# Kernel tuning notes

Hardware: AMD Instinct MI355X
Metric: run time of the kernel (lower is better)

Reference implementation:

```python
import jax, jax.numpy as jnp
import numpy as np
import math

BS, C, NH, NL, NP = 2, 128, 1, 2, 8
SHAPES = np.array([[128, 256], [64, 128]], dtype=np.int64)  # [num_level, (H, W)]
NQ = int(SHAPES[0, 0] * SHAPES[0, 1])  # 32768 queries at level-0 resolution
NV = int((SHAPES[:, 0] * SHAPES[:, 1]).sum())  # 40960


def _offset_bias():
    # replicate init_weights grid bias
    thetas = np.arange(NH, dtype=np.float32) * (2.0 * math.pi / NH)
    grid = np.stack([np.cos(thetas), np.sin(thetas)], -1)
    grid = grid / np.abs(grid).max(-1, keepdims=True)
    grid = np.tile(grid.reshape(NH, 1, 1, 2), (1, NL, NP, 1))
    for i in range(NP):
        grid[:, :, i, :] *= i + 1
    return jnp.asarray(grid.reshape(-1), dtype=jnp.float32)


def setup_inputs() -> dict:
    key = jax.random.key(0)
    ks = jax.random.split(key, 8)
    query = jax.random.normal(ks[0], (BS, NQ, C), dtype=jnp.float32)
    value = jax.random.normal(ks[1], (BS, NV, C), dtype=jnp.float32)
    query_location = jax.random.uniform(ks[2], (BS, NQ, NL, 2), dtype=jnp.float32)
    spatial_shapes = jnp.asarray(SHAPES)
    level_start_index = jnp.asarray(np.concatenate([[0], np.cumsum(SHAPES[:, 0] * SHAPES[:, 1])[:-1]]))
    # params (small random offset weights instead of exact-zero init so offsets depend on query)
    W_off = 0.01 * jax.random.normal(ks[3], (C, NH * NL * NP * 2), dtype=jnp.float32)
    b_off = _offset_bias()
    W_attn = 0.01 * jax.random.normal(ks[4], (C, NH * NL * NP), dtype=jnp.float32)
    b_attn = jnp.zeros((NH * NL * NP,), dtype=jnp.float32)
    lim = 1.0 / np.sqrt(C)
    W_out = jax.random.uniform(ks[5], (C * NH, C), minval=-lim, maxval=lim, dtype=jnp.float32)
    b_out = jnp.zeros((C,), dtype=jnp.float32)
    return {"query": query, "value": value, "query_location": query_location,
            "spatial_shapes": spatial_shapes, "level_start_index": level_start_index,
            "W_off": W_off, "b_off": b_off, "W_attn": W_attn, "b_attn": b_attn,
            "W_out": W_out, "b_out": b_out}


def _ms_deform_attn(value, shapes_np, loc, aw):
    # value: [bs, nv, c]; loc: [bs, nq, nh, nl, np, 2] in [0,1]; aw: [bs, nq, nh, nl, np]
    bs, nq = loc.shape[0], loc.shape[1]
    hd = value.shape[-1] // NH
    out = jnp.zeros((bs, NH, nq, hd), dtype=value.dtype)
    start = 0
    for l in range(NL):
        H, W = int(shapes_np[l, 0]), int(shapes_np[l, 1])
        # [bs, nh, H*W, hd]
        v = value[:, start:start + H * W].reshape(bs, H * W, NH, hd).transpose(0, 2, 1, 3)
        # grid_sample align_corners=False convention: x = gx*W - 0.5 with gx in [0,1]
        x = loc[:, :, :, l, :, 0] * W - 0.5  # [bs, nq, nh, np]
        y = loc[:, :, :, l, :, 1] * H - 0.5
        x0 = jnp.floor(x); y0 = jnp.floor(y)
        lx = (x - x0).transpose(0, 2, 1, 3).reshape(bs, NH, nq * NP)[..., None]
        ly = (y - y0).transpose(0, 2, 1, 3).reshape(bs, NH, nq * NP)[..., None]
        x0i = x0.astype(jnp.int32); y0i = y0.astype(jnp.int32)

        def gat(ix, iy):
            valid = ((ix >= 0) & (ix < W) & (iy >= 0) & (iy < H)).astype(value.dtype)
            idx = jnp.clip(iy, 0, H - 1) * W + jnp.clip(ix, 0, W - 1)
            idx_t = idx.transpose(0, 2, 1, 3).reshape(bs, NH, nq * NP)
            g = jnp.take_along_axis(v, idx_t[..., None], axis=2)  # [bs, nh, nq*np, hd]
            m = valid.transpose(0, 2, 1, 3).reshape(bs, NH, nq * NP)
            return g * m[..., None]

        samp = (gat(x0i, y0i) * (1 - lx) * (1 - ly)
                + gat(x0i + 1, y0i) * lx * (1 - ly)
                + gat(x0i, y0i + 1) * (1 - lx) * ly
                + gat(x0i + 1, y0i + 1) * lx * ly)  # [bs, nh, nq*np, hd]
        w = aw[:, :, :, l].transpose(0, 2, 1, 3).reshape(bs, NH, nq * NP)[..., None]
        out = out + (samp * w).reshape(bs, NH, nq, NP, hd).sum(3)
        start += H * W
    return out.transpose(0, 2, 1, 3).reshape(bs, nq, NH * hd)


def reference(query, value, query_location, spatial_shapes, level_start_index,
              W_off, b_off, W_attn, b_attn, W_out, b_out):
    bs, nq, c = query.shape
    shapes_np = np.asarray(spatial_shapes)
    off = (query @ W_off + b_off).reshape(bs, nq, NH, NL, NP, 2)
    aw = jax.nn.softmax((query @ W_attn + b_attn).reshape(bs, nq, NH, NL * NP), axis=-1)
    aw = aw.reshape(bs, nq, NH, NL, NP)
    # offset_normalizer = [W, H] per level
    norm = jnp.stack([jnp.asarray(shapes_np[:, 1], jnp.float32),
                      jnp.asarray(shapes_np[:, 0], jnp.float32)], -1)  # [nl, 2]
    loc = query_location[:, :, None, :, None, :] + off / norm[None, None, None, :, None, :]
    out = _ms_deform_attn(value, shapes_np, loc, aw)
    return out @ W_out + b_out  # dropout is identity at eval
```

## Files before the change

kernel.cpp:

```cpp
#include <hip/hip_runtime.h>
#include <hip/hip_fp16.h>


#define QB 32

struct __align__(8) h2x2 { __half2 a, b; };

typedef _Float16 f16x8 __attribute__((ext_vector_type(8)));
typedef _Float16 f16x4 __attribute__((ext_vector_type(4)));
typedef float    f32x4 __attribute__((ext_vector_type(4)));

__global__ __launch_bounds__(256) void cvt_value_f16_kernel(
    const float4* __restrict__ in, h2x2* __restrict__ out, int n4)
{
    const int i = blockIdx.x * 256 + threadIdx.x;
    if (i < n4) {
        const float4 f = in[i];
        h2x2 h;
        h.a = __floats2half2_rn(f.x, f.y);
        h.b = __floats2half2_rn(f.z, f.w);
        out[i] = h;
    }
}

__global__ __launch_bounds__(256) void wout_transpose_kernel(
    const float* __restrict__ Wout, _Float16* __restrict__ wTg)
{
    __shared__ float t[128 * 129];
    const int tid = threadIdx.x;
    #pragma unroll
    for (int i = 0; i < 16; ++i) {
        const int f  = tid + i * 256;
        const int k  = f >> 5;
        const int c4 = f & 31;
        const float4 v = ((const float4*)Wout)[k * 32 + c4];
        t[k * 129 + c4 * 4 + 0] = v.x;
        t[k * 129 + c4 * 4 + 1] = v.y;
        t[k * 129 + c4 * 4 + 2] = v.z;
        t[k * 129 + c4 * 4 + 3] = v.w;
    }
    __syncthreads();
    #pragma unroll
    for (int i = 0; i < 64; ++i) {
        const int f = tid + i * 256;
        const int n = f >> 7;
        const int k = f & 127;
        wTg[n * 128 + k] = (_Float16)t[k * 129 + n];
    }
}

#define MSDA_PROLOGUE                                                          \
    float* q_tile = (float*)smem_u;                                            \
    int4*  tab    = (int4*)smem_u;                                             \
    const int tid = threadIdx.x;                                               \
    const int r0  = blockIdx.x * QB;                                           \
    {                                                                          \
        const float4* src = (const float4*)query + (size_t)r0 * 32;            \
        float4* dst = (float4*)q_tile;                                         \
        _Pragma("unroll")                                                      \
        for (int i = 0; i < 4; ++i)                                            \
            dst[tid + i * 256] = src[tid + i * 256];                           \
    }                                                                          \
    __syncthreads();                                                           \
    {                                                                          \
        const int jo = tid & 31;                                               \
        const int qb = (tid >> 5) * 4;                                         \
        float s[4] = {0.f, 0.f, 0.f, 0.f};                                     \
        for (int c4 = 0; c4 < 32; ++c4) {                                      \
            const float w0 = Woff[(c4 * 4 + 0) * 32 + jo];                     \
            const float w1 = Woff[(c4 * 4 + 1) * 32 + jo];                     \
            const float w2 = Woff[(c4 * 4 + 2) * 32 + jo];                     \
            const float w3 = Woff[(c4 * 4 + 3) * 32 + jo];                     \
            _Pragma("unroll")                                                  \
            for (int k = 0; k < 4; ++k) {                                      \
                const float4 q4 = *(const float4*)&q_tile[(qb + k) * 128 + c4 * 4]; \
                s[k] += q4.x * w0 + q4.y * w1 + q4.z * w2 + q4.w * w3;         \
            }                                                                  \
        }                                                                      \
        const int l = jo >> 4;                                                 \
        const int d = jo & 1;                                                  \
        const float scale = (d == 0) ? (l == 0 ? 256.f : 128.f)                \
                                     : (l == 0 ? 128.f : 64.f);                \
        const float bo = boff[jo];                                             \
        _Pragma("unroll")                                                      \
        for (int k = 0; k < 4; ++k) {                                          \
            const int row = r0 + qb + k;                                       \
            const float ql = qloc[row * 4 + l * 2 + d];                        \
            coords[(qb + k) * 32 + jo] = ql * scale + (s[k] + bo) - 0.5f;      \
        }                                                                      \
    }                                                                          \
    {                                                                          \
        const int ja = tid & 15;                                               \
        const int qb = (tid >> 4) * 2;                                         \
        float s[2] = {0.f, 0.f};                                               \
        for (int c4 = 0; c4 < 32; ++c4) {                                      \
            const float w0 = Wattn[(c4 * 4 + 0) * 16 + ja];                    \
            const float w1 = Wattn[(c4 * 4 + 1) * 16 + ja];                    \
            const float w2 = Wattn[(c4 * 4 + 2) * 16 + ja];                    \
            const float w3 = Wattn[(c4 * 4 + 3) * 16 + ja];                    \
            _Pragma("unroll")                                                  \
            for (int k = 0; k < 2; ++k) {                                      \
                const float4 q4 = *(const float4*)&q_tile[(qb + k) * 128 + c4 * 4]; \
                s[k] += q4.x * w0 + q4.y * w1 + q4.z * w2 + q4.w * w3;         \
            }                                                                  \
        }                                                                      \
        const float ba = battn[ja];                                            \
        _Pragma("unroll")                                                      \
        for (int k = 0; k < 2; ++k)                                            \
            aws[(qb + k) * 16 + ja] = s[k] + ba;                               \
    }                                                                          \
    __syncthreads();                                                           \
    if (tid < QB) {                                                            \
        float* a = &aws[tid * 16];                                             \
        float m = a[0];                                                        \
        _Pragma("unroll")                                                      \
        for (int j = 1; j < 16; ++j) m = fmaxf(m, a[j]);                       \
        float sum = 0.f;                                                       \
        _Pragma("unroll")                                                      \
        for (int j = 0; j < 16; ++j) {                                         \
            const float e = __expf(a[j] - m);                                  \
            a[j] = e;                                                          \
            sum += e;                                                          \
        }                                                                      \
        const float r = 1.f / sum;                                             \
        _Pragma("unroll")                                                      \
        for (int j = 0; j < 16; ++j) a[j] *= r;                                \
    }                                                                          \
    __syncthreads();                                                           \
    _Pragma("unroll")                                                          \
    for (int e = tid; e < QB * 16; e += 256) {                                 \
        const int q = e >> 4;                                                  \
        const int p = e & 15;                                                  \
        const int l = p >> 3;                                                  \
        const int H = l ? 64 : 128;                                            \
        const int W = l ? 128 : 256;                                           \
        const int S = l ? 32768 : 0;                                           \
        const float x   = coords[q * 32 + p * 2 + 0];                          \
        const float y   = coords[q * 32 + p * 2 + 1];                          \
        const float wgt = aws[q * 16 + p];                                     \
        const float xf = floorf(x), yf = floorf(y);                            \
        const float lx = x - xf, ly = y - yf;                                  \
        const int x0 = (int)xf, y0 = (int)yf;                                  \
        const int x1 = x0 + 1, y1 = y0 + 1;                                    \
        const float hx = 1.f - lx, hy = 1.f - ly;                              \
        float w00 = wgt * hx * hy;                                             \
        float w10 = wgt * lx * hy;                                             \
        float w01 = wgt * hx * ly;                                             \
        float w11 = wgt * lx * ly;                                             \
        if (x0 < 0 || x0 >= W) { w00 = 0.f; w01 = 0.f; }                       \
        if (x1 < 0 || x1 >= W) { w10 = 0.f; w11 = 0.f; }                       \
        if (y0 < 0 || y0 >= H) { w00 = 0.f; w10 = 0.f; }                       \
        if (y1 < 0 || y1 >= H) { w01 = 0.f; w11 = 0.f; }                       \
        const int cx0 = min(max(x0, 0), W - 1);                                \
        const int cx1 = min(max(x1, 0), W - 1);                                \
        const int cy0 = min(max(y0, 0), H - 1);                                \
        const int cy1 = min(max(y1, 0), H - 1);                                \
        int4 e0, e1;                                                           \
        e0.x = __float_as_int(w00); e0.y = __float_as_int(w01);                \
        e0.z = (S + cy0 * W + cx0) * 32; e0.w = (S + cy1 * W + cx0) * 32;      \
        e1.x = __float_as_int(w10); e1.y = __float_as_int(w11);                \
        e1.z = (S + cy0 * W + cx1) * 32; e1.w = (S + cy1 * W + cx1) * 32;      \
        tab[e * 2]     = e0;                                                   \
        tab[e * 2 + 1] = e1;                                                   \
    }                                                                          \
    __syncthreads();

__global__ __launch_bounds__(256, 4) void msda_gather_f16_kernel(
    const float* __restrict__ query,
    const h2x2*  __restrict__ value_h,
    const float* __restrict__ qloc,
    const float* __restrict__ Woff,
    const float* __restrict__ boff,
    const float* __restrict__ Wattn,
    const float* __restrict__ battn,
    float* __restrict__ acc_out)
{
    __shared__ __align__(16) char smem_u[QB * 128 * 4];
    __shared__ float coords[QB * 32];
    __shared__ float aws[QB * 16];
    MSDA_PROLOGUE

    {
        const int wv   = tid >> 6;
        const int lane = tid & 63;
        const int half = lane >> 5;
        const int cl   = lane & 31;
        const h2x2* vb = value_h + (size_t)(blockIdx.x >> 10) * (40960 * 32);
        float4* og = (float4*)acc_out;

        #pragma unroll 1
        for (int i = 0; i < 8; ++i) {
            const int q = wv * 8 + i;
            float ax = 0.f, ay = 0.f, az = 0.f, aw4 = 0.f;

            #pragma unroll 1
            for (int p0 = 0; p0 < 16; p0 += 8) {
                float wa[8], wb[8];
                int   oa[8], ob[8];
                #pragma unroll
                for (int pi = 0; pi < 8; ++pi) {
                    const int4 t = tab[((q * 16 + p0 + pi) << 1) + half];
                    wa[pi] = __int_as_float(t.x);
                    wb[pi] = __int_as_float(t.y);
                    oa[pi] = t.z + cl;
                    ob[pi] = t.w + cl;
                }
                h2x2 vA[8], vB[8];
                #pragma unroll
                for (int pi = 0; pi < 8; ++pi) {
                    vA[pi] = vb[oa[pi]];
                    vB[pi] = vb[ob[pi]];
                }
                #pragma unroll
                for (int pi = 0; pi < 8; ++pi) {
                    ax  += wa[pi] * __low2float(vA[pi].a);
                    ay  += wa[pi] * __high2float(vA[pi].a);
                    az  += wa[pi] * __low2float(vA[pi].b);
                    aw4 += wa[pi] * __high2float(vA[pi].b);
                    ax  += wb[pi] * __low2float(vB[pi].a);
                    ay  += wb[pi] * __high2float(vB[pi].a);
                    az  += wb[pi] * __low2float(vB[pi].b);
                    aw4 += wb[pi] * __high2float(vB[pi].b);
                }
            }
            ax  += __shfl_xor(ax, 32, 64);
            ay  += __shfl_xor(ay, 32, 64);
            az  += __shfl_xor(az, 32, 64);
            aw4 += __shfl_xor(aw4, 32, 64);
            if (half == 0)
                og[(size_t)(r0 + q) * 32 + cl] = make_float4(ax, ay, az, aw4);
        }
    }
}

__global__ __launch_bounds__(256, 4) void msda_gather_f32_kernel(
    const float* __restrict__ query,
    const float* __restrict__ value,
    const float* __restrict__ qloc,
    const float* __restrict__ Woff,
    const float* __restrict__ boff,
    const float* __restrict__ Wattn,
    const float* __restrict__ battn,
    float* __restrict__ acc_out)
{
    __shared__ __align__(16) char smem_u[QB * 128 * 4];
    __shared__ float coords[QB * 32];
    __shared__ float aws[QB * 16];
    MSDA_PROLOGUE

    {
        const int wv   = tid >> 6;
        const int lane = tid & 63;
        const int half = lane >> 5;
        const int cl   = lane & 31;
        const float4* vb = (const float4*)value
                         + (size_t)(blockIdx.x >> 10) * (40960 * 32);
        float4* og = (float4*)acc_out;

        #pragma unroll 1
        for (int i = 0; i < 8; ++i) {
            const int q = wv * 8 + i;
            float ax = 0.f, ay = 0.f, az = 0.f, aw4 = 0.f;

            #pragma unroll 1
            for (int p0 = 0; p0 < 16; p0 += 8) {
                float wa[8], wb[8];
                int   oa[8], ob[8];
                #pragma unroll
                for (int pi = 0; pi < 8; ++pi) {
                    const int4 t = tab[((q * 16 + p0 + pi) << 1) + half];
                    wa[pi] = __int_as_float(t.x);
                    wb[pi] = __int_as_float(t.y);
                    oa[pi] = t.z + cl;
                    ob[pi] = t.w + cl;
                }
                float4 vA[8], vB[8];
                #pragma unroll
                for (int pi = 0; pi < 8; ++pi) {
                    vA[pi] = vb[oa[pi]];
                    vB[pi] = vb[ob[pi]];
                }
                #pragma unroll
                for (int pi = 0; pi < 8; ++pi) {
                    ax  += wa[pi] * vA[pi].x + wb[pi] * vB[pi].x;
                    ay  += wa[pi] * vA[pi].y + wb[pi] * vB[pi].y;
                    az  += wa[pi] * vA[pi].z + wb[pi] * vB[pi].z;
                    aw4 += wa[pi] * vA[pi].w + wb[pi] * vB[pi].w;
                }
            }
            ax  += __shfl_xor(ax, 32, 64);
            ay  += __shfl_xor(ay, 32, 64);
            az  += __shfl_xor(az, 32, 64);
            aw4 += __shfl_xor(aw4, 32, 64);
            if (half == 0)
                og[(size_t)(r0 + q) * 32 + cl] = make_float4(ax, ay, az, aw4);
        }
    }
}

__global__ __launch_bounds__(256, 2) void msda_out_gemm_mfma_kernel(
    const _Float16* __restrict__ wTg,
    const float* __restrict__ bout,
    float* __restrict__ out)
{
    __shared__ _Float16 aT[128 * 136];
    __shared__ _Float16 wT[128 * 136];
    const int tid = threadIdx.x;
    const int m0  = blockIdx.x * 128;

    #pragma unroll
    for (int i = 0; i < 8; ++i) {
        const int t  = tid + i * 256;
        const int n  = t >> 4;
        const int k8 = t & 15;
        *(f16x8*)&wT[n * 136 + k8 * 8] = *(const f16x8*)&wTg[n * 128 + k8 * 8];
    }
    {
        const float4* src = (const float4*)out;
        #pragma unroll
        for (int i = 0; i < 16; ++i) {
            const int t  = tid + i * 256;
            const int r  = t >> 5;
            const int c4 = t & 31;
            const float4 v = src[(size_t)(m0 + r) * 32 + c4];
            f16x4 h;
            h[0] = (_Float16)v.x; h[1] = (_Float16)v.y;
            h[2] = (_Float16)v.z; h[3] = (_Float16)v.w;
            *(f16x4*)&aT[r * 136 + c4 * 4] = h;
        }
    }
    __syncthreads();

    const int wv   = tid >> 6;
    const int lane = tid & 63;
    const int quad = lane >> 4;
    const int lr   = lane & 15;

    f32x4 acc_[2][8];
    #pragma unroll
    for (int mt = 0; mt < 2; ++mt)
        #pragma unroll
        for (int nt = 0; nt < 8; ++nt)
            acc_[mt][nt] = (f32x4){0.f, 0.f, 0.f, 0.f};

    #pragma unroll
    for (int k0 = 0; k0 < 128; k0 += 32) {
        const f16x8 a0 = *(const f16x8*)&aT[(wv * 32 +  0 + lr) * 136 + k0 + quad * 8];
        const f16x8 a1 = *(const f16x8*)&aT[(wv * 32 + 16 + lr) * 136 + k0 + quad * 8];
        #pragma unroll
        for (int nt = 0; nt < 8; ++nt) {
            const f16x8 b = *(const f16x8*)&wT[(nt * 16 + lr) * 136 + k0 + quad * 8];
            acc_[0][nt] = __builtin_amdgcn_mfma_f32_16x16x32_f16(a0, b, acc_[0][nt], 0, 0, 0);
            acc_[1][nt] = __builtin_amdgcn_mfma_f32_16x16x32_f16(a1, b, acc_[1][nt], 0, 0, 0);
        }
    }

    #pragma unroll
    for (int nt = 0; nt < 8; ++nt) {
        const float bb = bout[nt * 16 + lr];
        #pragma unroll
        for (int mt = 0; mt < 2; ++mt) {
            #pragma unroll
            for (int reg = 0; reg < 4; ++reg) {
                const int row = m0 + wv * 32 + mt * 16 + quad * 4 + reg;
                out[(size_t)row * 128 + nt * 16 + lr] = acc_[mt][nt][reg] + bb;
            }
        }
    }
}

#define GR 128
__global__ __launch_bounds__(256, 2) void msda_out_gemm_f32_kernel(
    const float* __restrict__ Wout,
    const float* __restrict__ bout,
    float* __restrict__ out)
{
    __shared__ __align__(16) float a_tile[GR * 68];
    __shared__ __align__(16) float w_tile[64 * 128];
    const int tid  = threadIdx.x;
    const int r0   = blockIdx.x * GR;
    const int trow = tid >> 4;
    const int tcol = tid & 15;

    float4 o[8][2];
    #pragma unroll
    for (int k = 0; k < 8; ++k) {
        o[k][0] = make_float4(0.f, 0.f, 0.f, 0.f);
        o[k][1] = make_float4(0.f, 0.f, 0.f, 0.f);
    }

    #pragma unroll 1
    for (int h = 0; h < 2; ++h) {
        {
            const float4* src = (const float4*)out;
            #pragma unroll
            for (int i = 0; i < 8; ++i) {
                const int t  = tid + i * 256;
                const int r  = t >> 4;
                const int c4 = t & 15;
                const float4 v = src[(size_t)(r0 + r) * 32 + h * 16 + c4];
                *(float4*)&a_tile[r * 68 + c4 * 4] = v;
            }
            const float4* ws = (const float4*)Wout + (size_t)h * 64 * 32;
            float4* wd = (float4*)w_tile;
            #pragma unroll
            for (int i = 0; i < 8; ++i)
                wd[tid + i * 256] = ws[tid + i * 256];
        }
        __syncthreads();

        #pragma unroll 1
        for (int c4 = 0; c4 < 16; ++c4) {
            float4 a4[8];
            #pragma unroll
            for (int k = 0; k < 8; ++k)
                a4[k] = *(const float4*)&a_tile[(trow + 16 * k) * 68 + c4 * 4];
            #pragma unroll
            for (int j = 0; j < 4; ++j) {
                const int ci = c4 * 4 + j;
                const float4 w0 = *(const float4*)&w_tile[ci * 128 + tcol * 4];
                const float4 w1 = *(const float4*)&w_tile[ci * 128 + 64 + tcol * 4];
                #pragma unroll
                for (int k = 0; k < 8; ++k) {
                    const float a = (j == 0) ? a4[k].x : (j == 1) ? a4[k].y
                                  : (j == 2) ? a4[k].z : a4[k].w;
                    o[k][0].x += a * w0.x; o[k][0].y += a * w0.y;
                    o[k][0].z += a * w0.z; o[k][0].w += a * w0.w;
                    o[k][1].x += a * w1.x; o[k][1].y += a * w1.y;
                    o[k][1].z += a * w1.z; o[k][1].w += a * w1.w;
                }
            }
        }
        __syncthreads();
    }

    const float4 b0 = ((const float4*)bout)[tcol];
    const float4 b1 = ((const float4*)bout)[16 + tcol];
    float4* og = (float4*)out;
    #pragma unroll
    for (int k = 0; k < 8; ++k) {
        const size_t row = (size_t)(r0 + trow + 16 * k);
        float4 v0 = o[k][0], v1 = o[k][1];
        v0.x += b0.x; v0.y += b0.y; v0.z += b0.z; v0.w += b0.w;
        v1.x += b1.x; v1.y += b1.y; v1.z += b1.z; v1.w += b1.w;
        og[row * 32 + tcol]      = v0;
        og[row * 32 + 16 + tcol] = v1;
    }
}

extern "C" void kernel_launch(void* const* d_in, const int* in_sizes, int n_in,
                              void* d_out, int out_size, void* d_ws, size_t ws_size,
                              hipStream_t stream) {
    const float* query = (const float*)d_in[0];
    const float* value = (const float*)d_in[1];
    const float* qloc  = (const float*)d_in[2];
    const float* Woff  = (const float*)d_in[5];
    const float* boff  = (const float*)d_in[6];
    const float* Wattn = (const float*)d_in[7];
    const float* battn = (const float*)d_in[8];
    const float* Wout  = (const float*)d_in[9];
    const float* bout  = (const float*)d_in[10];
    float* out = (float*)d_out;

    const int n_val = 2 * 40960 * 128;
    const size_t f16_bytes = (size_t)n_val * 2;
    const size_t wT_bytes  = 128 * 128 * 2;

    if (ws_size >= f16_bytes + wT_bytes) {
        h2x2* val16 = (h2x2*)d_ws;
        _Float16* wTg = (_Float16*)((char*)d_ws + f16_bytes);
        const int n4 = n_val / 4;
        hipLaunchKernelGGL(cvt_value_f16_kernel, dim3((n4 + 255) / 256), dim3(256),
                           0, stream, (const float4*)value, val16, n4);
        hipLaunchKernelGGL(wout_transpose_kernel, dim3(1), dim3(256), 0, stream,
                           Wout, wTg);
        hipLaunchKernelGGL(msda_gather_f16_kernel, dim3(65536 / QB), dim3(256),
                           0, stream,
                           query, (const h2x2*)val16, qloc, Woff, boff, Wattn, battn, out);
        hipLaunchKernelGGL(msda_out_gemm_mfma_kernel, dim3(65536 / 128), dim3(256),
                           0, stream, (const _Float16*)wTg, bout, out);
    } else if (ws_size >= f16_bytes) {
        h2x2* val16 = (h2x2*)d_ws;
        const int n4 = n_val / 4;
        hipLaunchKernelGGL(cvt_value_f16_kernel, dim3((n4 + 255) / 256), dim3(256),
                           0, stream, (const float4*)value, val16, n4);
        hipLaunchKernelGGL(msda_gather_f16_kernel, dim3(65536 / QB), dim3(256),
                           0, stream,
                           query, (const h2x2*)val16, qloc, Woff, boff, Wattn, battn, out);
        hipLaunchKernelGGL(msda_out_gemm_f32_kernel, dim3(65536 / GR), dim3(256),
                           0, stream, Wout, bout, out);
    } else {
        hipLaunchKernelGGL(msda_gather_f32_kernel, dim3(65536 / QB), dim3(256),
                           0, stream,
                           query, value, qloc, Woff, boff, Wattn, battn, out);
        hipLaunchKernelGGL(msda_out_gemm_f32_kernel, dim3(65536 / GR), dim3(256),
                           0, stream, Wout, bout, out);
    }
}
```

Baseline: 225.6 us.

## Fuse offset, attention-logit and softmax projections into one register pass with shuffles

```diff
diff --git a/kernel.cpp b/kernel.cpp
--- a/kernel.cpp
+++ b/kernel.cpp
@@ -63,109 +63,96 @@
     }                                                                          \
     __syncthreads();                                                           \
     {                                                                          \
-        const int jo = tid & 31;                                               \
-        const int qb = (tid >> 5) * 4;                                         \
-        float s[4] = {0.f, 0.f, 0.f, 0.f};                                     \
+        const int qg  = tid >> 4;                   \
+        const int p   = tid & 15;                      \
+        const int l   = p >> 3;                                                \
+        const int pin = p & 7;                                                 \
+        const int jx  = l * 16 + pin * 2;      \
+        float sx[2] = {0.f, 0.f}, sy[2] = {0.f, 0.f}, sa[2] = {0.f, 0.f};      \
         for (int c4 = 0; c4 < 32; ++c4) {                                      \
-            const float w0 = Woff[(c4 * 4 + 0) * 32 + jo];                     \
-            const float w1 = Woff[(c4 * 4 + 1) * 32 + jo];                     \
-            const float w2 = Woff[(c4 * 4 + 2) * 32 + jo];                     \
-            const float w3 = Woff[(c4 * 4 + 3) * 32 + jo];                     \
+            float2 wxy[4]; float wat[4];                                       \
             _Pragma("unroll")                                                  \
-            for (int k = 0; k < 4; ++k) {                                      \
-                const float4 q4 = *(const float4*)&q_tile[(qb + k) * 128 + c4 * 4]; \
-                s[k] += q4.x * w0 + q4.y * w1 + q4.z * w2 + q4.w * w3;         \
+            for (int r = 0; r < 4; ++r) {                                      \
+                wxy[r] = *(const float2*)&Woff[(c4 * 4 + r) * 32 + jx];        \
+                wat[r] = Wattn[(c4 * 4 + r) * 16 + p];                         \
+            }                                                                  \
+            _Pragma("unroll")                                                  \
+            for (int k = 0; k < 2; ++k) {                                      \
+                const float4 q4 = *(const float4*)&q_tile[(qg * 2 + k) * 128 + c4 * 4]; \
+                sx[k] += q4.x * wxy[0].x + q4.y * wxy[1].x                     \
+                       + q4.z * wxy[2].x + q4.w * wxy[3].x;                    \
+                sy[k] += q4.x * wxy[0].y + q4.y * wxy[1].y                     \
+                       + q4.z * wxy[2].y + q4.w * wxy[3].y;                    \
+                sa[k] += q4.x * wat[0] + q4.y * wat[1]                         \
+                       + q4.z * wat[2] + q4.w * wat[3];                        \
             }                                                                  \
         }                                                                      \
-        const int l = jo >> 4;                                                 \
-        const int d = jo & 1;                                                  \
-        const float scale = (d == 0) ? (l == 0 ? 256.f : 128.f)                \
-                                     : (l == 0 ? 128.f : 64.f);                \
-        const float bo = boff[jo];                                             \
+        const float Wf = l ? 128.f : 256.f;                                    \
+        const float Hf = l ? 64.f : 128.f;                                     \
+        const float box = boff[jx], boy = boff[jx + 1];                        \
+        const float ba  = battn[p];                                            \
+        float xx[2], yy[2], lg[2];                                             \
         _Pragma("unroll")                                                      \
-        for (int k = 0; k < 4; ++k) {                                          \
-            const int row = r0 + qb + k;                                       \
-            const float ql = qloc[row * 4 + l * 2 + d];                        \
-            coords[(qb + k) * 32 + jo] = ql * scale + (s[k] + bo) - 0.5f;      \
+        for (int k = 0; k < 2; ++k) {                                          \
+            const int row = r0 + qg * 2 + k;                                   \
+            xx[k] = qloc[row * 4 + l * 2 + 0] * Wf + (sx[k] + box) - 0.5f;     \
+            yy[k] = qloc[row * 4 + l * 2 + 1] * Hf + (sy[k] + boy) - 0.5f;     \
+            lg[k] = sa[k] + ba;                                                \
+        }                                                                      \
+                  \
+        float m0 = lg[0], m1 = lg[1];                                          \
+        _Pragma("unroll")                                                      \
+        for (int s_ = 1; s_ < 16; s_ <<= 1) {                                  \
+            m0 = fmaxf(m0, __shfl_xor(m0, s_, 64));                            \
+            m1 = fmaxf(m1, __shfl_xor(m1, s_, 64));                            \
+        }                                                                      \
+        float ex0 = __expf(lg[0] - m0), ex1 = __expf(lg[1] - m1);              \
+        float sm0 = ex0, sm1 = ex1;                                            \
+        _Pragma("unroll")                                                      \
+        for (int s_ = 1; s_ < 16; s_ <<= 1) {                                  \
+            sm0 += __shfl_xor(sm0, s_, 64);                                    \
+            sm1 += __shfl_xor(sm1, s_, 64);                                    \
+        }                                                                      \
+        const float wgt_[2] = {ex0 / sm0, ex1 / sm1};                          \
+        __syncthreads();    \
+        const int Hi = l ? 64 : 128;                                           \
+        const int Wi = l ? 128 : 256;                                          \
+        const int S  = l ? 32768 : 0;                                          \
+        _Pragma("unroll")                                                      \
+        for (int k = 0; k < 2; ++k) {                                          \
+            const int q = qg * 2 + k;                                          \
+            const float x = xx[k], y = yy[k];                                  \
+            const float wgt = wgt_[k];                                         \
+            const float xf = floorf(x), yf = floorf(y);                        \
+            const float lx = x - xf, ly = y - yf;                              \
+            const int x0 = (int)xf, y0 = (int)yf;                              \
+            const int x1 = x0 + 1, y1 = y0 + 1;                                \
+            const float hx = 1.f - lx, hy = 1.f - ly;                          \
+            float w00 = wgt * hx * hy;                                         \
+            float w10 = wgt * lx * hy;                                         \
+            float w01 = wgt * hx * ly;                                         \
+            float w11 = wgt * lx * ly;                                         \
+            if (x0 < 0 || x0 >= Wi) { w00 = 0.f; w01 = 0.f; }                  \
+            if (x1 < 0 || x1 >= Wi) { w10 = 0.f; w11 = 0.f; }                  \
+            if (y0 < 0 || y0 >= Hi) { w00 = 0.f; w10 = 0.f; }                  \
+            if (y1 < 0 || y1 >= Hi) { w01 = 0.f; w11 = 0.f; }                  \
+            const int cx0 = min(max(x0, 0), Wi - 1);                           \
+            const int cx1 = min(max(x1, 0), Wi - 1);                           \
+            const int cy0 = min(max(y0, 0), Hi - 1);                           \
+            const int cy1 = min(max(y1, 0), Hi - 1);                           \
+            int4 e0i, e1i;                                                     \
+            e0i.x = __float_as_int(w00); e0i.y = __float_as_int(w01);          \
+            e0i.z = (S + cy0 * Wi + cx0) * 32; e0i.w = (S + cy1 * Wi + cx0) * 32; \
+            e1i.x = __float_as_int(w10); e1i.y = __float_as_int(w11);          \
+            e1i.z = (S + cy0 * Wi + cx1) * 32; e1i.w = (S + cy1 * Wi + cx1) * 32; \
+            const int e_ = q * 16 + p;                                         \
+            tab[e_ * 2]     = e0i;                                             \
+            tab[e_ * 2 + 1] = e1i;                                             \
         }                                                                      \
     }                                                                          \
-    {                                                                          \
-        const int ja = tid & 15;                                               \
-        const int qb = (tid >> 4) * 2;                                         \
-        float s[2] = {0.f, 0.f};                                               \
-        for (int c4 = 0; c4 < 32; ++c4) {                                      \
-            const float w0 = Wattn[(c4 * 4 + 0) * 16 + ja];                    \
-            const float w1 = Wattn[(c4 * 4 + 1) * 16 + ja];                    \
-            const float w2 = Wattn[(c4 * 4 + 2) * 16 + ja];                    \
-            const float w3 = Wattn[(c4 * 4 + 3) * 16 + ja];                    \
-            _Pragma("unroll")                                                  \
-            for (int k = 0; k < 2; ++k) {                                      \
-                const float4 q4 = *(const float4*)&q_tile[(qb + k) * 128 + c4 * 4]; \
-                s[k] += q4.x * w0 + q4.y * w1 + q4.z * w2 + q4.w * w3;         \
-            }                                                                  \
-        }                                                                      \
-        const float ba = battn[ja];                                            \
-        _Pragma("unroll")                                                      \
-        for (int k = 0; k < 2; ++k)                                            \
-            aws[(qb + k) * 16 + ja] = s[k] + ba;                               \
-    }                                                                          \
-    __syncthreads();                                                           \
-    if (tid < QB) {                                                            \
-        float* a = &aws[tid * 16];                                             \
-        float m = a[0];                                                        \
-        _Pragma("unroll")                                                      \
-        for (int j = 1; j < 16; ++j) m = fmaxf(m, a[j]);                       \
-        float sum = 0.f;                                                       \
-        _Pragma("unroll")                                                      \
-        for (int j = 0; j < 16; ++j) {                                         \
-            const float e = __expf(a[j] - m);                                  \
-            a[j] = e;                                                          \
-            sum += e;                                                          \
-        }                                                                      \
-        const float r = 1.f / sum;                                             \
-        _Pragma("unroll")                                                      \
-        for (int j = 0; j < 16; ++j) a[j] *= r;                                \
-    }                                                                          \
-    __syncthreads();                                                           \
-    _Pragma("unroll")                                                          \
-    for (int e = tid; e < QB * 16; e += 256) {                                 \
-        const int q = e >> 4;                                                  \
-        const int p = e & 15;                                                  \
-        const int l = p >> 3;                                                  \
-        const int H = l ? 64 : 128;                                            \
-        const int W = l ? 128 : 256;                                           \
-        const int S = l ? 32768 : 0;                                           \
-        const float x   = coords[q * 32 + p * 2 + 0];                          \
-        const float y   = coords[q * 32 + p * 2 + 1];                          \
-        const float wgt = aws[q * 16 + p];                                     \
-        const float xf = floorf(x), yf = floorf(y);                            \
-        const float lx = x - xf, ly = y - yf;                                  \
-        const int x0 = (int)xf, y0 = (int)yf;                                  \
-        const int x1 = x0 + 1, y1 = y0 + 1;                                    \
-        const float hx = 1.f - lx, hy = 1.f - ly;                              \
-        float w00 = wgt * hx * hy;                                             \
-        float w10 = wgt * lx * hy;                                             \
-        float w01 = wgt * hx * ly;                                             \
-        float w11 = wgt * lx * ly;                                             \
-        if (x0 < 0 || x0 >= W) { w00 = 0.f; w01 = 0.f; }                       \
-        if (x1 < 0 || x1 >= W) { w10 = 0.f; w11 = 0.f; }                       \
-        if (y0 < 0 || y0 >= H) { w00 = 0.f; w10 = 0.f; }                       \
-        if (y1 < 0 || y1 >= H) { w01 = 0.f; w11 = 0.f; }                       \
-        const int cx0 = min(max(x0, 0), W - 1);                                \
-        const int cx1 = min(max(x1, 0), W - 1);                                \
-        const int cy0 = min(max(y0, 0), H - 1);                                \
-        const int cy1 = min(max(y1, 0), H - 1);                                \
-        int4 e0, e1;                                                           \
-        e0.x = __float_as_int(w00); e0.y = __float_as_int(w01);                \
-        e0.z = (S + cy0 * W + cx0) * 32; e0.w = (S + cy1 * W + cx0) * 32;      \
-        e1.x = __float_as_int(w10); e1.y = __float_as_int(w11);                \
-        e1.z = (S + cy0 * W + cx1) * 32; e1.w = (S + cy1 * W + cx1) * 32;      \
-        tab[e * 2]     = e0;                                                   \
-        tab[e * 2 + 1] = e1;                                                   \
-    }                                                                          \
     __syncthreads();
 
-__global__ __launch_bounds__(256, 4) void msda_gather_f16_kernel(
+__global__ __launch_bounds__(256, 8) void msda_gather_f16_kernel(
     const float* __restrict__ query,
     const h2x2*  __restrict__ value_h,
     const float* __restrict__ qloc,
@@ -176,8 +163,6 @@
     float* __restrict__ acc_out)
 {
     __shared__ __align__(16) char smem_u[QB * 128 * 4];
-    __shared__ float coords[QB * 32];
-    __shared__ float aws[QB * 16];
     MSDA_PROLOGUE
 
     {
@@ -233,7 +218,7 @@
     }
 }
 
-__global__ __launch_bounds__(256, 4) void msda_gather_f32_kernel(
+__global__ __launch_bounds__(256, 8) void msda_gather_f32_kernel(
     const float* __restrict__ query,
     const float* __restrict__ value,
     const float* __restrict__ qloc,
@@ -244,8 +229,6 @@
     float* __restrict__ acc_out)
 {
     __shared__ __align__(16) char smem_u[QB * 128 * 4];
-    __shared__ float coords[QB * 32];
-    __shared__ float aws[QB * 16];
     MSDA_PROLOGUE
 
     {
```

Measured after the change: 246.6 us. 9.3% more time.
